# Kernel optimization log

Hardware: AMD Instinct MI355X
Metric: run time of the kernel (lower is better)

The kernel has to match this reference:

```python
import jax, jax.numpy as jnp
import numpy as np

N_HEAD = 16  # matches init_kwargs
LN_EPS = 1e-5


def setup_inputs() -> dict:
    key = jax.random.key(0)
    k0, k1, k2 = jax.random.split(key, 3)
    S, B, D = 2048, 2, 1024
    N, Dh = N_HEAD, D // N_HEAD
    h = jax.random.normal(k0, (S, B, D), dtype=jnp.float32)
    # causal mask, True = masked; source's dim==3 branch: shape [qlen, klen, batch]
    causal = jnp.triu(jnp.ones((S, S), dtype=bool), k=1)
    attn_mask = jnp.broadcast_to(causal[:, :, None], (S, S, B))
    W_qkv = jax.random.normal(k1, (D, 3 * N * Dh), dtype=jnp.float32) * (1.0 / np.sqrt(D))
    W_o = jax.random.normal(k2, (N * Dh, D), dtype=jnp.float32) * (1.0 / np.sqrt(N * Dh))
    gamma = jnp.ones((D,), dtype=jnp.float32)
    beta = jnp.zeros((D,), dtype=jnp.float32)
    return {"h": h, "attn_mask": attn_mask, "W_qkv": W_qkv, "W_o": W_o,
            "gamma": gamma, "beta": beta}


def reference(h, attn_mask, W_qkv, W_o, gamma, beta):
    # h: [S, B, D] (seq, batch, d_model) -- Transformer-XL layout
    S, B, D = h.shape
    N = N_HEAD
    Dh = W_o.shape[0] // N
    scale = 1.0 / np.sqrt(Dh)

    qkv = h @ W_qkv                                   # [S, B, 3*N*Dh]
    q, k, v = jnp.split(qkv, 3, axis=-1)
    q = q.reshape(S, B, N, Dh)
    k = k.reshape(S, B, N, Dh)
    v = v.reshape(S, B, N, Dh)

    # attention scores: [i, j, b, n]
    score = jnp.einsum('ibnd,jbnd->ijbn', q, k) * scale
    # mask (dim==3 branch of source): attn_mask [i, j, b] -> [i, j, b, 1]
    score = jnp.where(attn_mask[:, :, :, None], -jnp.inf, score)
    prob = jax.nn.softmax(score, axis=1)              # softmax over key axis j

    attn_vec = jnp.einsum('ijbn,jbnd->ibnd', prob, v).reshape(S, B, N * Dh)
    attn_out = attn_vec @ W_o                         # [S, B, D]

    # residual + LayerNorm (biased variance, like torch.nn.LayerNorm)
    x = h + attn_out
    mu = jnp.mean(x, axis=-1, keepdims=True)
    var = jnp.mean(jnp.square(x - mu), axis=-1, keepdims=True)
    out = (x - mu) * jax.lax.rsqrt(var + LN_EPS) * gamma + beta
    return out
```

## Files before the change

kernel.cpp:

```cpp
#include <hip/hip_runtime.h>

typedef unsigned short u16;
typedef unsigned int u32;
typedef __attribute__((ext_vector_type(8))) __bf16 bf16x8;
typedef __attribute__((ext_vector_type(4))) float f32x4;
typedef __attribute__((ext_vector_type(8))) unsigned short u16x8;
typedef __attribute__((ext_vector_type(4))) unsigned short u16x4;
typedef __attribute__((ext_vector_type(2))) unsigned int u32x2;
typedef __attribute__((ext_vector_type(4))) unsigned int u32x4;

#if defined(__has_builtin)
#if __has_builtin(__builtin_amdgcn_permlane32_swap) && __has_builtin(__builtin_amdgcn_permlane16_swap)
#define USE_PERMLANE 1
#endif
#endif
#ifndef USE_PERMLANE
#define USE_PERMLANE 0
#endif

__device__ __forceinline__ u16 f2bf(float f) {
    u32 u = __builtin_bit_cast(u32, f);
    u += 0x7fffu + ((u >> 16) & 1u);
    return (u16)(u >> 16);
}

__device__ __forceinline__ float fexp2(float x) {
#if __has_builtin(__builtin_amdgcn_exp2f)
    return __builtin_amdgcn_exp2f(x);
#else
    return exp2f(x);
#endif
}

__device__ __forceinline__ float frcp(float x) {
#if __has_builtin(__builtin_amdgcn_rcpf)
    return __builtin_amdgcn_rcpf(x);
#else
    return 1.0f / x;
#endif
}

__global__ __launch_bounds__(256) void conv_h_kernel(const float* __restrict__ h,
                                                     u16* __restrict__ hb) {
    int i = blockIdx.x * 256 + threadIdx.x;
    float4 v = ((const float4*)h)[i];
    u16x4 o = { f2bf(v.x), f2bf(v.y), f2bf(v.z), f2bf(v.w) };
    ((u16x4*)hb)[i] = o;
}

__global__ __launch_bounds__(256) void conv_wt_kernel(const float* __restrict__ W,
                                                      u16* __restrict__ Wt,
                                                      int R, int C,
                                                      int scale_rows, float scale) {
    __shared__ float tile[32][33];
    int t = threadIdx.x;
    int r = t >> 3, c4 = (t & 7) * 4;
    int gx = blockIdx.x * 32, gy = blockIdx.y * 32;
    float4 v = *(const float4*)&W[(size_t)(gy + r) * C + gx + c4];
    tile[r][c4 + 0] = v.x; tile[r][c4 + 1] = v.y;
    tile[r][c4 + 2] = v.z; tile[r][c4 + 3] = v.w;
    __syncthreads();
    float sc = (gx + r < scale_rows) ? scale : 1.0f;
    u16x4 o = { f2bf(tile[c4 + 0][r] * sc), f2bf(tile[c4 + 1][r] * sc),
                f2bf(tile[c4 + 2][r] * sc), f2bf(tile[c4 + 3][r] * sc) };
    *(u16x4*)&Wt[(size_t)(gx + r) * R + gy + c4] = o;
}

template <int MODE>
__global__ __launch_bounds__(256) void gemm_bt_kernel(
        const u16* __restrict__ A, const u16* __restrict__ Bt,
        u16* __restrict__ Cb, const float* __restrict__ H, float* __restrict__ X,
        int M, int N, int K) {
    constexpr int LDT = 40;
    __shared__ u16 alds[2][128 * LDT];
    __shared__ u16 blds[2][128 * LDT];
    const int t = threadIdx.x;
    const int lane = t & 63;
    const int wave = t >> 6;
    const int wm = wave >> 1, wn = wave & 1;
    const int m0 = blockIdx.x * 128;
    const int n0 = blockIdx.y * 128;
    const int nk = K >> 5;

    const int srow = t >> 1;
    const int sch = (t & 1) * 2;
    const u16* ga = A + (size_t)(m0 + srow) * K + sch * 8;
    const u16* gb = Bt + (size_t)(n0 + srow) * K + sch * 8;
    const int wo = srow * LDT + sch * 8;

    u16x8 ra0 = *(const u16x8*)(ga);
    u16x8 ra1 = *(const u16x8*)(ga + 8);
    u16x8 rb0 = *(const u16x8*)(gb);
    u16x8 rb1 = *(const u16x8*)(gb + 8);
    *(u16x8*)&alds[0][wo] = ra0;  *(u16x8*)&alds[0][wo + 8] = ra1;
    *(u16x8*)&blds[0][wo] = rb0;  *(u16x8*)&blds[0][wo + 8] = rb1;

    f32x4 acc[4][4] = {};
    const int ko = (lane >> 4) * 8;
    const int arow_base = wm * 64 + (lane & 15);
    const int brow_base = wn * 64 + (lane & 15);

    int cur = 0;
    for (int kt = 0; kt < nk; ++kt) {
        __syncthreads();
        if (kt + 1 < nk) {
            const u16* gan = ga + (kt + 1) * 32;
            const u16* gbn = gb + (kt + 1) * 32;
            ra0 = *(const u16x8*)(gan);
            ra1 = *(const u16x8*)(gan + 8);
            rb0 = *(const u16x8*)(gbn);
            rb1 = *(const u16x8*)(gbn + 8);
        }
        bf16x8 afrag[4], bfrag[4];
#pragma unroll
        for (int m = 0; m < 4; ++m)
            afrag[m] = *(const bf16x8*)&alds[cur][(arow_base + m * 16) * LDT + ko];
#pragma unroll
        for (int n = 0; n < 4; ++n)
            bfrag[n] = *(const bf16x8*)&blds[cur][(brow_base + n * 16) * LDT + ko];
#pragma unroll
        for (int m = 0; m < 4; ++m)
#pragma unroll
            for (int n = 0; n < 4; ++n)
                acc[m][n] = __builtin_amdgcn_mfma_f32_16x16x32_bf16(afrag[m], bfrag[n],
                                                                   acc[m][n], 0, 0, 0);
        if (kt + 1 < nk) {
            *(u16x8*)&alds[cur ^ 1][wo] = ra0;  *(u16x8*)&alds[cur ^ 1][wo + 8] = ra1;
            *(u16x8*)&blds[cur ^ 1][wo] = rb0;  *(u16x8*)&blds[cur ^ 1][wo + 8] = rb1;
        }
        cur ^= 1;
    }

#pragma unroll
    for (int m = 0; m < 4; ++m)
#pragma unroll
        for (int n = 0; n < 4; ++n)
#pragma unroll
            for (int r = 0; r < 4; ++r) {
                int row = m0 + wm * 64 + m * 16 + (lane >> 4) * 4 + r;
                int col = n0 + wn * 64 + n * 16 + (lane & 15);
                size_t idx = (size_t)row * N + col;
                if (MODE == 0) Cb[idx] = f2bf(acc[m][n][r]);
                else           X[idx] = acc[m][n][r] + H[idx];
            }
}

__global__ __launch_bounds__(256) void transpose_v_kernel(const u16* __restrict__ qkvb,
                                                          u16* __restrict__ vt) {
    __shared__ u16 tl[64][72];
    const int t = threadIdx.x;
    const int p = blockIdx.y;
    const int nn = p >> 1, b = p & 1;
    const int s0 = blockIdx.x * 64;
    const int r = t >> 2;
    const int ch = (t & 3) * 2;
    const u16* g = qkvb + ((size_t)(s0 + r) * 2 + b) * 3072 + 2048 + nn * 64;
    *(u16x8*)&tl[r][ch * 8]     = *(const u16x8*)(g + ch * 8);
    *(u16x8*)&tl[r][ch * 8 + 8] = *(const u16x8*)(g + ch * 8 + 8);
    __syncthreads();
    const int dh = t >> 2;
    const int sc = (t & 3) * 2;
    u16* o = vt + ((size_t)p * 64 + dh) * 2048 + s0;
#pragma unroll
    for (int q = 0; q < 2; ++q) {
        int scq = sc + q;
        u16x8 v;
#pragma unroll
        for (int j = 0; j < 8; ++j) v[j] = tl[scq * 8 + j][dh];
        *(u16x8*)(o + scq * 8) = v;
    }
}

__global__ __launch_bounds__(512) void attn_kernel(const u16* __restrict__ qkvb,
                                                   const u16* __restrict__ vt,
                                                   u16* __restrict__ attnb) {
    constexpr int LKT = 72;
    __shared__ u16 kvs[2][2][2][64 * LKT];
#if !USE_PERMLANE
    __shared__ u16 plds[8][16 * LKT];
#endif
    const int t = threadIdx.x;
    const int lane = t & 63;
    const int w = (t >> 6) & 3;
    const int grp = t >> 8;
    const int bid = blockIdx.x;
    const int qt = 31 - (bid >> 5);
    const int p = bid & 31;
    const int nn = p >> 1, b = p & 1;
    const int i0 = qt * 64;

    const int li = lane & 15;
    const int lg = lane >> 4;

    const int qrow = i0 + w * 16 + li;
    const u16* qg = qkvb + ((size_t)qrow * 2 + b) * 3072 + nn * 64 + lg * 8;
    bf16x8 qa0 = *(const bf16x8*)(qg);
    bf16x8 qa1 = *(const bf16x8*)(qg + 32);

    f32x4 o[4] = {};
    float mrun = -3.0e38f;
    float lrun = 0.f;

    const int tg = t & 255;
    const int srow = tg >> 2;
    const int sch = (tg & 3) * 2;
    const u16* kg = qkvb + 1024 + nn * 64 + sch * 8;
    const u16* vg = vt + ((size_t)p * 64 + srow) * 2048 + sch * 8;
    const int swo = srow * LKT + sch * 8;

    const int nt = qt + 1;
    const int G = (nt + 1) >> 1;

    u16x8 k0, k1, v0, v1;
    if (grp < nt) {
        const u16* kgp = kg + ((size_t)(grp * 64 + srow) * 2 + b) * 3072;
        k0 = *(const u16x8*)(kgp);  k1 = *(const u16x8*)(kgp + 8);
        const u16* vgp = vg + grp * 64;
        v0 = *(const u16x8*)(vgp);  v1 = *(const u16x8*)(vgp + 8);
        *(u16x8*)&kvs[grp][0][0][swo] = k0;  *(u16x8*)&kvs[grp][0][0][swo + 8] = k1;
        *(u16x8*)&kvs[grp][0][1][swo] = v0;  *(u16x8*)&kvs[grp][0][1][swo + 8] = v1;
    }
    __syncthreads();

    for (int s = 0; s < G; ++s) {
        const int jt = 2 * s + grp;
        const int buf = s & 1;
        const bool active = jt < nt;
        if (jt + 2 < nt) {
            const u16* kgp = kg + ((size_t)((jt + 2) * 64 + srow) * 2 + b) * 3072;
            k0 = *(const u16x8*)(kgp);  k1 = *(const u16x8*)(kgp + 8);
            const u16* vgp = vg + (jt + 2) * 64;
            v0 = *(const u16x8*)(vgp);  v1 = *(const u16x8*)(vgp + 8);
        }

        if (active) {
            const u16* kl = &kvs[grp][buf][0][0];
            const u16* vl = &kvs[grp][buf][1][0];

            f32x4 st[4];
            __builtin_amdgcn_s_setprio(1);
#pragma unroll
            for (int cf = 0; cf < 4; ++cf) {
                bf16x8 kb0 = *(const bf16x8*)&kl[(cf * 16 + li) * LKT + lg * 8];
                bf16x8 kb1 = *(const bf16x8*)&kl[(cf * 16 + li) * LKT + 32 + lg * 8];
                f32x4 z = {};
                z = __builtin_amdgcn_mfma_f32_16x16x32_bf16(kb0, qa0, z, 0, 0, 0);
                z = __builtin_amdgcn_mfma_f32_16x16x32_bf16(kb1, qa1, z, 0, 0, 0);
                st[cf] = z;
            }
            __builtin_amdgcn_s_setprio(0);

            if (jt == qt) {
                const int it = w * 16 + li;
#pragma unroll
                for (int cf = 0; cf < 4; ++cf)
#pragma unroll
                    for (int r = 0; r < 4; ++r) {
                        int jl = cf * 16 + lg * 4 + r;
                        if (jl > it) st[cf][r] = -3.0e38f;
                    }
            }

            float mloc = st[0][0];
#pragma unroll
            for (int cf = 0; cf < 4; ++cf)
#pragma unroll
                for (int r = 0; r < 4; ++r) mloc = fmaxf(mloc, st[cf][r]);
            mloc = fmaxf(mloc, __shfl_xor(mloc, 16, 64));
            mloc = fmaxf(mloc, __shfl_xor(mloc, 32, 64));

            if (__any(mloc > mrun + 8.0f)) {
                float mnew = fmaxf(mrun, mloc);
                float alpha = fexp2(mrun - mnew);
                lrun *= alpha;
                mrun = mnew;
#pragma unroll
                for (int r = 0; r < 4; ++r) {
                    float ar = __shfl(alpha, lg * 4 + r, 64);
#pragma unroll
                    for (int cf = 0; cf < 4; ++cf) o[cf][r] *= ar;
                }
            }

#if USE_PERMLANE
            float rsum = 0.f;
            u32 wv[4][2];
#pragma unroll
            for (int cf = 0; cf < 4; ++cf)
#pragma unroll
                for (int rr = 0; rr < 2; ++rr) {
                    float p0 = fexp2(st[cf][2 * rr] - mrun);
                    float p1 = fexp2(st[cf][2 * rr + 1] - mrun);
                    rsum += p0 + p1;
                    u32 wres;
                    asm("v_cvt_pk_bf16_f32 %0, %1, %2" : "=v"(wres) : "v"(p0), "v"(p1));
                    wv[cf][rr] = wres;
                }
            rsum += __shfl_xor(rsum, 16, 64);
            rsum += __shfl_xor(rsum, 32, 64);
            lrun += rsum;

            __builtin_amdgcn_s_setprio(1);
#pragma unroll
            for (int ks = 0; ks < 2; ++ks) {
                u32x2 sa = __builtin_amdgcn_permlane32_swap(wv[2 * ks][0], wv[2 * ks + 1][0], false, false);
                u32x2 fa = __builtin_amdgcn_permlane16_swap(sa[0], sa[1], false, false);
                u32x2 sb = __builtin_amdgcn_permlane32_swap(wv[2 * ks][1], wv[2 * ks + 1][1], false, false);
                u32x2 fb = __builtin_amdgcn_permlane16_swap(sb[0], sb[1], false, false);
                u32x4 fw = { fa[0], fb[0], fa[1], fb[1] };
                bf16x8 pa = __builtin_bit_cast(bf16x8, fw);
#pragma unroll
                for (int cf = 0; cf < 4; ++cf) {
                    bf16x8 vb = *(const bf16x8*)&vl[(cf * 16 + li) * LKT + ks * 32 + lg * 8];
                    o[cf] = __builtin_amdgcn_mfma_f32_16x16x32_bf16(pa, vb, o[cf], 0, 0, 0);
                }
            }
            __builtin_amdgcn_s_setprio(0);
#else
            float rsum = 0.f;
#pragma unroll
            for (int cf = 0; cf < 4; ++cf) {
                u16x4 pw;
#pragma unroll
                for (int r = 0; r < 4; ++r) {
                    float pv = fexp2(st[cf][r] - mrun);
                    rsum += pv;
                    pw[r] = f2bf(pv);
                }
                *(u16x4*)&plds[t >> 6][li * LKT + cf * 16 + lg * 4] = pw;
            }
            rsum += __shfl_xor(rsum, 16, 64);
            rsum += __shfl_xor(rsum, 32, 64);
            lrun += rsum;

            asm volatile("s_waitcnt lgkmcnt(0)" ::: "memory");
            __builtin_amdgcn_sched_barrier(0);

#pragma unroll
            for (int ks = 0; ks < 2; ++ks) {
                bf16x8 pa = *(const bf16x8*)&plds[t >> 6][li * LKT + ks * 32 + lg * 8];
#pragma unroll
                for (int cf = 0; cf < 4; ++cf) {
                    bf16x8 vb = *(const bf16x8*)&vl[(cf * 16 + li) * LKT + ks * 32 + lg * 8];
                    o[cf] = __builtin_amdgcn_mfma_f32_16x16x32_bf16(pa, vb, o[cf], 0, 0, 0);
                }
            }
#endif
        }

        if (jt + 2 < nt) {
            *(u16x8*)&kvs[grp][buf ^ 1][0][swo] = k0;  *(u16x8*)&kvs[grp][buf ^ 1][0][swo + 8] = k1;
            *(u16x8*)&kvs[grp][buf ^ 1][1][swo] = v0;  *(u16x8*)&kvs[grp][buf ^ 1][1][swo + 8] = v1;
        }
        __syncthreads();
    }

    float* osc = (float*)&kvs[1][0][0][0];
    float* msc = osc + 64 * 65;
    float* lsc = msc + 64;
    if (grp == 1) {
#pragma unroll
        for (int cf = 0; cf < 4; ++cf)
#pragma unroll
            for (int r = 0; r < 4; ++r)
                osc[(w * 16 + lg * 4 + r) * 65 + cf * 16 + li] = o[cf][r];
        if (lg == 0) { msc[w * 16 + li] = mrun; lsc[w * 16 + li] = lrun; }
    }
    __syncthreads();
    if (grp == 0) {
        float mB = msc[w * 16 + li];
        float lB = lsc[w * 16 + li];
        float m = fmaxf(mrun, mB);
        float eA = fexp2(mrun - m);
        float eB = fexp2(mB - m);
        float linv = frcp(lrun * eA + lB * eB);
#pragma unroll
        for (int r = 0; r < 4; ++r) {
            float eAr = __shfl(eA, lg * 4 + r, 64);
            float eBr = __shfl(eB, lg * 4 + r, 64);
            float rvr = __shfl(linv, lg * 4 + r, 64);
            int row = i0 + w * 16 + lg * 4 + r;
            u16* og = attnb + ((size_t)row * 2 + b) * 1024 + nn * 64;
#pragma unroll
            for (int cf = 0; cf < 4; ++cf) {
                float ob = osc[(w * 16 + lg * 4 + r) * 65 + cf * 16 + li];
                og[cf * 16 + li] = f2bf((o[cf][r] * eAr + ob * eBr) * rvr);
            }
        }
    }
}

__global__ __launch_bounds__(256) void ln_kernel(const float* __restrict__ X,
                                                 const float* __restrict__ gamma,
                                                 const float* __restrict__ beta,
                                                 float* __restrict__ out) {
    __shared__ float red[8];
    const int t = threadIdx.x;
    const int row = blockIdx.x;
    float4 v = ((const float4*)(X + (size_t)row * 1024))[t];
    float s = v.x + v.y + v.z + v.w;
#pragma unroll
    for (int off = 1; off < 64; off <<= 1) s += __shfl_xor(s, off, 64);
    if ((t & 63) == 0) red[t >> 6] = s;
    __syncthreads();
    float mu = (red[0] + red[1] + red[2] + red[3]) * (1.f / 1024.f);
    float dx = v.x - mu, dy = v.y - mu, dz = v.z - mu, dw = v.w - mu;
    float q = dx * dx + dy * dy + dz * dz + dw * dw;
#pragma unroll
    for (int off = 1; off < 64; off <<= 1) q += __shfl_xor(q, off, 64);
    if ((t & 63) == 0) red[4 + (t >> 6)] = q;
    __syncthreads();
    float var = (red[4] + red[5] + red[6] + red[7]) * (1.f / 1024.f);
    float rs = rsqrtf(var + 1e-5f);
    float4 g = ((const float4*)gamma)[t];
    float4 bt = ((const float4*)beta)[t];
    float4 o;
    o.x = dx * rs * g.x + bt.x;
    o.y = dy * rs * g.y + bt.y;
    o.z = dz * rs * g.z + bt.z;
    o.w = dw * rs * g.w + bt.w;
    ((float4*)(out + (size_t)row * 1024))[t] = o;
}

extern "C" void kernel_launch(void* const* d_in, const int* in_sizes, int n_in,
                              void* d_out, int out_size, void* d_ws, size_t ws_size,
                              hipStream_t stream) {
    const float* h     = (const float*)d_in[0];
    const float* Wqkv  = (const float*)d_in[2];
    const float* Wo    = (const float*)d_in[3];
    const float* gamma = (const float*)d_in[4];
    const float* beta  = (const float*)d_in[5];
    float* out = (float*)d_out;

    char* ws = (char*)d_ws;
    u16*   hb    = (u16*)(ws);
    u16*   wqkvt = (u16*)(ws + 8388608);
    u16*   wot   = (u16*)(ws + 14680064);
    u16*   qkvb  = (u16*)(ws + 16777216);
    u16*   vt    = (u16*)(ws + 41943040);
    u16*   attnb = (u16*)(ws + 50331648);
    float* xbuf  = (float*)(ws + 58720256);

    const float qscale = 0.125f * 1.44269504088896f;

    conv_h_kernel<<<4096, 256, 0, stream>>>(h, hb);
    conv_wt_kernel<<<dim3(96, 32), 256, 0, stream>>>(Wqkv, wqkvt, 1024, 3072, 1024, qscale);
    conv_wt_kernel<<<dim3(32, 32), 256, 0, stream>>>(Wo, wot, 1024, 1024, 0, 1.0f);
    gemm_bt_kernel<0><<<dim3(32, 24), 256, 0, stream>>>(hb, wqkvt, qkvb, nullptr, nullptr,
                                                        4096, 3072, 1024);
    transpose_v_kernel<<<dim3(32, 32), 256, 0, stream>>>(qkvb, vt);
    attn_kernel<<<1024, 512, 0, stream>>>(qkvb, vt, attnb);
    gemm_bt_kernel<1><<<dim3(32, 8), 256, 0, stream>>>(attnb, wot, nullptr, h, xbuf,
                                                       4096, 1024, 1024);
    ln_kernel<<<4096, 256, 0, stream>>>(xbuf, gamma, beta, out);
}
```

Before: 117.3 us.

## Use 32x32x16 MFMA with 128-row query tiles in causal attention

```diff
diff --git a/kernel.cpp b/kernel.cpp
--- a/kernel.cpp
+++ b/kernel.cpp
@@ -4,19 +4,11 @@
 typedef unsigned int u32;
 typedef __attribute__((ext_vector_type(8))) __bf16 bf16x8;
 typedef __attribute__((ext_vector_type(4))) float f32x4;
+typedef __attribute__((ext_vector_type(16))) float f32x16;
 typedef __attribute__((ext_vector_type(8))) unsigned short u16x8;
 typedef __attribute__((ext_vector_type(4))) unsigned short u16x4;
 typedef __attribute__((ext_vector_type(2))) unsigned int u32x2;
 typedef __attribute__((ext_vector_type(4))) unsigned int u32x4;
-
-#if defined(__has_builtin)
-#if __has_builtin(__builtin_amdgcn_permlane32_swap) && __has_builtin(__builtin_amdgcn_permlane16_swap)
-#define USE_PERMLANE 1
-#endif
-#endif
-#ifndef USE_PERMLANE
-#define USE_PERMLANE 0
-#endif
 
 __device__ __forceinline__ u16 f2bf(float f) {
     u32 u = __builtin_bit_cast(u32, f);
@@ -171,33 +163,35 @@
     }
 }
 
-__global__ __launch_bounds__(512) void attn_kernel(const u16* __restrict__ qkvb,
-                                                   const u16* __restrict__ vt,
-                                                   u16* __restrict__ attnb) {
+__global__ __launch_bounds__(512, 4) void attn_kernel(const u16* __restrict__ qkvb,
+                                                      const u16* __restrict__ vt,
+                                                      u16* __restrict__ attnb) {
     constexpr int LKT = 72;
     __shared__ u16 kvs[2][2][2][64 * LKT];
-#if !USE_PERMLANE
-    __shared__ u16 plds[8][16 * LKT];
-#endif
     const int t = threadIdx.x;
     const int lane = t & 63;
     const int w = (t >> 6) & 3;
     const int grp = t >> 8;
     const int bid = blockIdx.x;
-    const int qt = 31 - (bid >> 5);
+    const int g = bid >> 5;
+    const int qt = (g < 8) ? (15 - g) : (g - 8);
     const int p = bid & 31;
     const int nn = p >> 1, b = p & 1;
-    const int i0 = qt * 64;
-
-    const int li = lane & 15;
-    const int lg = lane >> 4;
-
-    const int qrow = i0 + w * 16 + li;
-    const u16* qg = qkvb + ((size_t)qrow * 2 + b) * 3072 + nn * 64 + lg * 8;
-    bf16x8 qa0 = *(const bf16x8*)(qg);
-    bf16x8 qa1 = *(const bf16x8*)(qg + 32);
-
-    f32x4 o[4] = {};
+    const int i0 = qt * 128;
+
+    const int il = lane & 31;
+    const int hi = lane >> 5;
+
+    bf16x8 qa[4];
+    {
+        const u16* qg = qkvb + ((size_t)(i0 + w * 32 + il) * 2 + b) * 3072
+                        + nn * 64 + hi * 8;
+#pragma unroll
+        for (int kc = 0; kc < 4; ++kc)
+            qa[kc] = *(const bf16x8*)(qg + kc * 16);
+    }
+
+    f32x16 o[2] = {};
     float mrun = -3.0e38f;
     float lrun = 0.f;
 
@@ -208,11 +202,11 @@
     const u16* vg = vt + ((size_t)p * 64 + srow) * 2048 + sch * 8;
     const int swo = srow * LKT + sch * 8;
 
-    const int nt = qt + 1;
-    const int G = (nt + 1) >> 1;
+    const int nt = 2 * qt + 2;
+    const int G = nt >> 1;
 
     u16x8 k0, k1, v0, v1;
-    if (grp < nt) {
+    {
         const u16* kgp = kg + ((size_t)(grp * 64 + srow) * 2 + b) * 3072;
         k0 = *(const u16x8*)(kgp);  k1 = *(const u16x8*)(kgp + 8);
         const u16* vgp = vg + grp * 64;
@@ -225,7 +219,6 @@
     for (int s = 0; s < G; ++s) {
         const int jt = 2 * s + grp;
         const int buf = s & 1;
-        const bool active = jt < nt;
         if (jt + 2 < nt) {
             const u16* kgp = kg + ((size_t)((jt + 2) * 64 + srow) * 2 + b) * 3072;
             k0 = *(const u16x8*)(kgp);  k1 = *(const u16x8*)(kgp + 8);
@@ -233,40 +226,41 @@
             v0 = *(const u16x8*)(vgp);  v1 = *(const u16x8*)(vgp + 8);
         }
 
-        if (active) {
+        const bool skip = (jt * 64 > i0 + w * 32 + 31);
+        if (!skip) {
             const u16* kl = &kvs[grp][buf][0][0];
             const u16* vl = &kvs[grp][buf][1][0];
 
-            f32x4 st[4];
+            f32x16 st[2];
             __builtin_amdgcn_s_setprio(1);
 #pragma unroll
-            for (int cf = 0; cf < 4; ++cf) {
-                bf16x8 kb0 = *(const bf16x8*)&kl[(cf * 16 + li) * LKT + lg * 8];
-                bf16x8 kb1 = *(const bf16x8*)&kl[(cf * 16 + li) * LKT + 32 + lg * 8];
-                f32x4 z = {};
-                z = __builtin_amdgcn_mfma_f32_16x16x32_bf16(kb0, qa0, z, 0, 0, 0);
-                z = __builtin_amdgcn_mfma_f32_16x16x32_bf16(kb1, qa1, z, 0, 0, 0);
-                st[cf] = z;
+            for (int jc = 0; jc < 2; ++jc) {
+                f32x16 z = {};
+#pragma unroll
+                for (int kc = 0; kc < 4; ++kc) {
+                    bf16x8 kb = *(const bf16x8*)&kl[(jc * 32 + il) * LKT + kc * 16 + hi * 8];
+                    z = __builtin_amdgcn_mfma_f32_32x32x16_bf16(kb, qa[kc], z, 0, 0, 0);
+                }
+                st[jc] = z;
             }
             __builtin_amdgcn_s_setprio(0);
 
-            if (jt == qt) {
-                const int it = w * 16 + li;
-#pragma unroll
-                for (int cf = 0; cf < 4; ++cf)
-#pragma unroll
-                    for (int r = 0; r < 4; ++r) {
-                        int jl = cf * 16 + lg * 4 + r;
-                        if (jl > it) st[cf][r] = -3.0e38f;
+            if (jt * 64 + 63 > i0 + w * 32) {
+                const int iglob = i0 + w * 32 + il;
+#pragma unroll
+                for (int jc = 0; jc < 2; ++jc)
+#pragma unroll
+                    for (int r = 0; r < 16; ++r) {
+                        int jglob = jt * 64 + jc * 32 + (r & 3) + 8 * (r >> 2) + 4 * hi;
+                        if (jglob > iglob) st[jc][r] = -3.0e38f;
                     }
             }
 
             float mloc = st[0][0];
 #pragma unroll
-            for (int cf = 0; cf < 4; ++cf)
-#pragma unroll
-                for (int r = 0; r < 4; ++r) mloc = fmaxf(mloc, st[cf][r]);
-            mloc = fmaxf(mloc, __shfl_xor(mloc, 16, 64));
+            for (int jc = 0; jc < 2; ++jc)
+#pragma unroll
+                for (int r = 0; r < 16; ++r) mloc = fmaxf(mloc, st[jc][r]);
             mloc = fmaxf(mloc, __shfl_xor(mloc, 32, 64));
 
             if (__any(mloc > mrun + 8.0f)) {
@@ -275,77 +269,46 @@
                 lrun *= alpha;
                 mrun = mnew;
 #pragma unroll
-                for (int r = 0; r < 4; ++r) {
-                    float ar = __shfl(alpha, lg * 4 + r, 64);
-#pragma unroll
-                    for (int cf = 0; cf < 4; ++cf) o[cf][r] *= ar;
+                for (int r = 0; r < 16; ++r) {
+                    float ar = __shfl(alpha, (r & 3) + 8 * (r >> 2) + 4 * hi, 64);
+                    o[0][r] *= ar;
+                    o[1][r] *= ar;
                 }
             }
 
-#if USE_PERMLANE
             float rsum = 0.f;
-            u32 wv[4][2];
-#pragma unroll
-            for (int cf = 0; cf < 4; ++cf)
-#pragma unroll
-                for (int rr = 0; rr < 2; ++rr) {
-                    float p0 = fexp2(st[cf][2 * rr] - mrun);
-                    float p1 = fexp2(st[cf][2 * rr + 1] - mrun);
-                    rsum += p0 + p1;
-                    u32 wres;
-                    asm("v_cvt_pk_bf16_f32 %0, %1, %2" : "=v"(wres) : "v"(p0), "v"(p1));
-                    wv[cf][rr] = wres;
+#pragma unroll
+            for (int jc = 0; jc < 2; ++jc) {
+                u32 W[4][2];
+#pragma unroll
+                for (int gg = 0; gg < 4; ++gg)
+#pragma unroll
+                    for (int u = 0; u < 2; ++u) {
+                        float p0 = fexp2(st[jc][4 * gg + 2 * u] - mrun);
+                        float p1 = fexp2(st[jc][4 * gg + 2 * u + 1] - mrun);
+                        rsum += p0 + p1;
+                        u32 wres;
+                        asm("v_cvt_pk_bf16_f32 %0, %1, %2" : "=v"(wres) : "v"(p0), "v"(p1));
+                        W[gg][u] = wres;
+                    }
+                __builtin_amdgcn_s_setprio(1);
+#pragma unroll
+                for (int jk = 0; jk < 2; ++jk) {
+                    u32x2 s0 = __builtin_amdgcn_permlane32_swap(W[2 * jk][0], W[2 * jk + 1][0], false, false);
+                    u32x2 s1 = __builtin_amdgcn_permlane32_swap(W[2 * jk][1], W[2 * jk + 1][1], false, false);
+                    u32x4 fw = { s0[0], s1[0], s0[1], s1[1] };
+                    bf16x8 pa = __builtin_bit_cast(bf16x8, fw);
+#pragma unroll
+                    for (int cf = 0; cf < 2; ++cf) {
+                        bf16x8 vb = *(const bf16x8*)&vl[(cf * 32 + il) * LKT
+                                                        + jc * 32 + jk * 16 + hi * 8];
+                        o[cf] = __builtin_amdgcn_mfma_f32_32x32x16_bf16(pa, vb, o[cf], 0, 0, 0);
+                    }
                 }
-            rsum += __shfl_xor(rsum, 16, 64);
+                __builtin_amdgcn_s_setprio(0);
+            }
             rsum += __shfl_xor(rsum, 32, 64);
             lrun += rsum;
-
-            __builtin_amdgcn_s_setprio(1);
-#pragma unroll
-            for (int ks = 0; ks < 2; ++ks) {
-                u32x2 sa = __builtin_amdgcn_permlane32_swap(wv[2 * ks][0], wv[2 * ks + 1][0], false, false);
-                u32x2 fa = __builtin_amdgcn_permlane16_swap(sa[0], sa[1], false, false);
-                u32x2 sb = __builtin_amdgcn_permlane32_swap(wv[2 * ks][1], wv[2 * ks + 1][1], false, false);
-                u32x2 fb = __builtin_amdgcn_permlane16_swap(sb[0], sb[1], false, false);
-                u32x4 fw = { fa[0], fb[0], fa[1], fb[1] };
-                bf16x8 pa = __builtin_bit_cast(bf16x8, fw);
-#pragma unroll
-                for (int cf = 0; cf < 4; ++cf) {
-                    bf16x8 vb = *(const bf16x8*)&vl[(cf * 16 + li) * LKT + ks * 32 + lg * 8];
-                    o[cf] = __builtin_amdgcn_mfma_f32_16x16x32_bf16(pa, vb, o[cf], 0, 0, 0);
-                }
-            }
-            __builtin_amdgcn_s_setprio(0);
-#else
-            float rsum = 0.f;
-#pragma unroll
-            for (int cf = 0; cf < 4; ++cf) {
-                u16x4 pw;
-#pragma unroll
-                for (int r = 0; r < 4; ++r) {
-                    float pv = fexp2(st[cf][r] - mrun);
-                    rsum += pv;
-                    pw[r] = f2bf(pv);
-                }
-                *(u16x4*)&plds[t >> 6][li * LKT + cf * 16 + lg * 4] = pw;
-            }
-            rsum += __shfl_xor(rsum, 16, 64);
-            rsum += __shfl_xor(rsum, 32, 64);
-            lrun += rsum;
-
-            asm volatile("s_waitcnt lgkmcnt(0)" ::: "memory");
-            __builtin_amdgcn_sched_barrier(0);
-
-#pragma unroll
-            for (int ks = 0; ks < 2; ++ks) {
-                bf16x8 pa = *(const bf16x8*)&plds[t >> 6][li * LKT + ks * 32 + lg * 8];
-#pragma unroll
-                for (int cf = 0; cf < 4; ++cf) {
-                    bf16x8 vb = *(const bf16x8*)&vl[(cf * 16 + li) * LKT + ks * 32 + lg * 8];
-                    o[cf] = __builtin_amdgcn_mfma_f32_16x16x32_bf16(pa, vb, o[cf], 0, 0, 0);
-                }
-            }
-#endif
         }
 
         if (jt + 2 < nt) {
@@ -356,35 +319,38 @@
     }
 
     float* osc = (float*)&kvs[1][0][0][0];
-    float* msc = osc + 64 * 65;
-    float* lsc = msc + 64;
+    float* msc = osc + 128 * 65;
+    float* lsc = msc + 128;
     if (grp == 1) {
 #pragma unroll
-        for (int cf = 0; cf < 4; ++cf)
-#pragma unroll
-            for (int r = 0; r < 4; ++r)
-                osc[(w * 16 + lg * 4 + r) * 65 + cf * 16 + li] = o[cf][r];
-        if (lg == 0) { msc[w * 16 + li] = mrun; lsc[w * 16 + li] = lrun; }
+        for (int cf = 0; cf < 2; ++cf)
+#pragma unroll
+            for (int r = 0; r < 16; ++r) {
+                int iL = (r & 3) + 8 * (r >> 2) + 4 * hi;
+                osc[(w * 32 + iL) * 65 + cf * 32 + il] = o[cf][r];
+            }
+        if (hi == 0) { msc[w * 32 + il] = mrun; lsc[w * 32 + il] = lrun; }
     }
     __syncthreads();
     if (grp == 0) {
-        float mB = msc[w * 16 + li];
-        float lB = lsc[w * 16 + li];
+        float mB = msc[w * 32 + il];
+        float lB = lsc[w * 32 + il];
         float m = fmaxf(mrun, mB);
         float eA = fexp2(mrun - m);
         float eB = fexp2(mB - m);
         float linv = frcp(lrun * eA + lB * eB);
 #pragma unroll
-        for (int r = 0; r < 4; ++r) {
-            float eAr = __shfl(eA, lg * 4 + r, 64);
-            float eBr = __shfl(eB, lg * 4 + r, 64);
-            float rvr = __shfl(linv, lg * 4 + r, 64);
-            int row = i0 + w * 16 + lg * 4 + r;
+        for (int r = 0; r < 16; ++r) {
+            int iL = (r & 3) + 8 * (r >> 2) + 4 * hi;
+            float eAr = __shfl(eA, iL, 64);
+            float eBr = __shfl(eB, iL, 64);
+            float rvr = __shfl(linv, iL, 64);
+            int row = i0 + w * 32 + iL;
             u16* og = attnb + ((size_t)row * 2 + b) * 1024 + nn * 64;
 #pragma unroll
-            for (int cf = 0; cf < 4; ++cf) {
-                float ob = osc[(w * 16 + lg * 4 + r) * 65 + cf * 16 + li];
-                og[cf * 16 + li] = f2bf((o[cf][r] * eAr + ob * eBr) * rvr);
+            for (int cf = 0; cf < 2; ++cf) {
+                float ob = osc[(w * 32 + iL) * 65 + cf * 32 + il];
+                og[cf * 32 + il] = f2bf((o[cf][r] * eAr + ob * eBr) * rvr);
             }
         }
     }
@@ -449,7 +415,7 @@
     gemm_bt_kernel<0><<<dim3(32, 24), 256, 0, stream>>>(hb, wqkvt, qkvb, nullptr, nullptr,
                                                         4096, 3072, 1024);
     transpose_v_kernel<<<dim3(32, 32), 256, 0, stream>>>(qkvb, vt);
-    attn_kernel<<<1024, 512, 0, stream>>>(qkvb, vt, attnb);
+    attn_kernel<<<512, 512, 0, stream>>>(qkvb, vt, attnb);
     gemm_bt_kernel<1><<<dim3(32, 8), 256, 0, stream>>>(attnb, wot, nullptr, h, xbuf,
                                                        4096, 1024, 1024);
     ln_kernel<<<4096, 256, 0, stream>>>(xbuf, gamma, beta, out);
```

After: 122.9 us. +4.7%, slower.
